# Kernel tuning notes

Measured on AMD Instinct MI355X. Metric: run time of the kernel, lower is better.

The kernel has to match this reference:

```python
import jax
import jax.numpy as jnp
from jax import lax
import numpy as np

# ---- static RPN config (mirrors init_kwargs) ----
STRIDES = (8, 16)
SIZES = ((32, 32), (16, 16))
SCALES = ((64.0 ** 2,), (128.0 ** 2,))
RATIOS = ((0.5, 1.0, 2.0), (0.5, 1.0, 2.0))
IMAGE_SIZE = (256, 256)
NMS_THRESH = 0.7
POST_NMS_TOP_N = 2000
NUM_LEVELS = 2
TOP_K_PER_LEVEL = POST_NMS_TOP_N // NUM_LEVELS  # padded NMS output slots per level


def _generate_anchors(stride, scales, ratios, size, image_size):
    """Anchors of shape (H*W*A, 4) in (x1,y1,x2,y2), clamped to image."""
    H, W = size
    cy = (np.arange(H, dtype=np.float32) + 0.5) * stride
    cx = (np.arange(W, dtype=np.float32) + 0.5) * stride
    ws, hs = [], []
    for s in scales:
        for r in ratios:
            ws.append(np.sqrt(s / r))
            hs.append(np.sqrt(s * r))
    ws = np.asarray(ws, np.float32)  # [A]
    hs = np.asarray(hs, np.float32)
    cxg, cyg = np.meshgrid(cx, cy)  # [H, W]
    x1 = cxg[..., None] - 0.5 * ws
    y1 = cyg[..., None] - 0.5 * hs
    x2 = cxg[..., None] + 0.5 * ws
    y2 = cyg[..., None] + 0.5 * hs
    a = np.stack([x1, y1, x2, y2], axis=-1)  # [H, W, A, 4]
    a[..., 0] = np.clip(a[..., 0], 0, image_size[0])
    a[..., 1] = np.clip(a[..., 1], 0, image_size[1])
    a[..., 2] = np.clip(a[..., 2], 0, image_size[0])
    a[..., 3] = np.clip(a[..., 3], 0, image_size[1])
    return a.reshape(-1, 4).astype(np.float32)


ANCHORS = [
    _generate_anchors(STRIDES[i], SCALES[i], RATIOS[i], SIZES[i], IMAGE_SIZE)
    for i in range(NUM_LEVELS)
]


def conv2d(x, w, b, padding):
    y = lax.conv_general_dilated(
        x, w, window_strides=(1, 1), padding=padding,
        dimension_numbers=("NCHW", "OIHW", "NCHW"))
    return y + b[None, :, None, None]


def decode_boxes(anchors, deltas):
    """Standard R-CNN box decode. anchors [N,4], deltas [..., N, 4]."""
    wa = anchors[:, 2] - anchors[:, 0]
    ha = anchors[:, 3] - anchors[:, 1]
    cxa = anchors[:, 0] + 0.5 * wa
    cya = anchors[:, 1] + 0.5 * ha
    dx, dy, dw, dh = deltas[..., 0], deltas[..., 1], deltas[..., 2], deltas[..., 3]
    cx = dx * wa + cxa
    cy = dy * ha + cya
    w = jnp.exp(dw) * wa
    h = jnp.exp(dh) * ha
    return jnp.stack([cx - 0.5 * w, cy - 0.5 * h, cx + 0.5 * w, cy + 0.5 * h], axis=-1)


def clamp_boxes(b):
    return jnp.stack([
        jnp.clip(b[..., 0], 0.0, IMAGE_SIZE[0]),
        jnp.clip(b[..., 1], 0.0, IMAGE_SIZE[1]),
        jnp.clip(b[..., 2], 0.0, IMAGE_SIZE[0]),
        jnp.clip(b[..., 3], 0.0, IMAGE_SIZE[1]),
    ], axis=-1)


def _pairwise_iou(b):
    # b: [N, 4] -> [N, N] IoU (torchvision convention, no +1)
    area = (b[:, 2] - b[:, 0]) * (b[:, 3] - b[:, 1])
    lt = jnp.maximum(b[:, None, :2], b[None, :, :2])
    rb = jnp.minimum(b[:, None, 2:], b[None, :, 2:])
    wh = jnp.clip(rb - lt, 0.0)
    inter = wh[..., 0] * wh[..., 1]
    return inter / (area[:, None] + area[None, :] - inter)


def nms_padded(boxes, scores, thresh, top_k):
    """Exact greedy NMS; returns (top_k,4) boxes and (top_k,) scores padded with -1."""
    N = boxes.shape[0]
    order = jnp.argsort(-scores)
    b = boxes[order]
    s = scores[order]
    iou = _pairwise_iou(b)  # [N, N]

    def body(supp, xs):
        row, i = xs
        keep_i = jnp.logical_not(supp[i])
        supp = supp | (keep_i & (row > thresh) & (jnp.arange(N) > i))
        return supp, keep_i

    _, keep = lax.scan(body, jnp.zeros((N,), bool), (iou, jnp.arange(N)))
    rank = jnp.cumsum(keep) - 1  # position among kept, in score order
    slot = jnp.where(keep & (rank < top_k), rank, top_k)  # overflow -> dump row
    out_b = jnp.full((top_k + 1, 4), -1.0, boxes.dtype).at[slot].set(b)
    out_s = jnp.full((top_k + 1,), -1.0, scores.dtype).at[slot].set(s)
    return out_b[:top_k], out_s[:top_k]


def _rpn_level(feat, anchors, conv_w, conv_b, cls_w, cls_b, reg_w, reg_b):
    x = jax.nn.relu(conv2d(feat, conv_w, conv_b, "SAME"))
    cls = conv2d(x, cls_w, cls_b, "VALID")              # [BS, A, H, W]
    reg = conv2d(x, reg_w, reg_b, "VALID")              # [BS, 4A, H, W]
    BS, A, H, W = cls.shape
    cls = cls.transpose(0, 2, 3, 1).reshape(BS, -1)                      # [BS, HWA]
    reg = reg.transpose(0, 2, 3, 1).reshape(BS, H, W, A, 4).reshape(BS, -1, 4)
    boxes = clamp_boxes(decode_boxes(anchors, lax.stop_gradient(reg)))   # [BS, HWA, 4]
    scores = jax.nn.sigmoid(lax.stop_gradient(cls))                      # [BS, HWA]
    kb, ks = jax.vmap(lambda bb, ss: nms_padded(bb, ss, NMS_THRESH, TOP_K_PER_LEVEL))(boxes, scores)
    return kb, ks


def setup_inputs() -> dict:
    key = jax.random.key(0)
    ks = jax.random.split(key, 5)
    C = 256
    A = 3
    return {
        "feat0": jax.random.normal(ks[0], (4, C, 32, 32), jnp.float32),
        "feat1": jax.random.normal(ks[1], (4, C, 16, 16), jnp.float32),
        "conv_w": 0.01 * jax.random.normal(ks[2], (C, C, 3, 3), jnp.float32),
        "conv_b": jnp.zeros((C,), jnp.float32),
        "cls_w": 0.01 * jax.random.normal(ks[3], (A, C, 1, 1), jnp.float32),
        "cls_b": jnp.zeros((A,), jnp.float32),
        "reg_w": 0.01 * jax.random.normal(ks[4], (4 * A, C, 1, 1), jnp.float32),
        "reg_b": jnp.zeros((4 * A,), jnp.float32),
    }


def reference(feat0, feat1, conv_w, conv_b, cls_w, cls_b, reg_w, reg_b):
    feats = [feat0, feat1]
    kb_all, ks_all = [], []
    for i in range(NUM_LEVELS):
        kb, ks = _rpn_level(feats[i], jnp.asarray(ANCHORS[i]),
                            conv_w, conv_b, cls_w, cls_b, reg_w, reg_b)
        kb_all.append(kb)
        ks_all.append(ks)
    bboxes = jnp.concatenate(kb_all, axis=1)   # [BS, POST_NMS_TOP_N, 4]
    scores = jnp.concatenate(ks_all, axis=1)   # [BS, POST_NMS_TOP_N]
    idx = jnp.argsort(-scores, axis=1)         # descending; -1 pads go last
    bboxes = jnp.take_along_axis(bboxes, idx[..., None], axis=1)
    return bboxes
```

## Files before the change

### kernel.cpp

```cpp
#include <hip/hip_runtime.h>
#include <math.h>


__global__ __launch_bounds__(256, 4) void conv3_sk_u(
    const float* __restrict__ feat0, const float* __restrict__ feat1,
    const float* __restrict__ conv_w,
    double* __restrict__ part0, double* __restrict__ part1)
{
  __shared__ float Ald[2][16][64];
  __shared__ float Bld[2][16][64];
  const int t = threadIdx.x;
  const int bid = blockIdx.x;
  const float* feat;
  double* part;
  int oc_t, p_t, k_base, hw_sh, w_sh, H;
  if (bid < 1024) {
    int kc = bid >> 8;
    feat = feat0; part = part0 + (size_t)kc * 4096 * 256;
    oc_t = bid & 3; p_t = (bid >> 2) & 63;
    k_base = kc * 576; hw_sh = 10; w_sh = 5; H = 32;
  } else {
    int b2 = bid - 1024;
    int kc = b2 >> 6;
    feat = feat1; part = part1 + (size_t)kc * 1024 * 256;
    oc_t = b2 & 3; p_t = (b2 >> 2) & 15;
    k_base = kc * 576; hw_sh = 8; w_sh = 4; H = 16;
  }
  const int oc_base = oc_t * 64;
  const int p_base  = p_t * 64;
  const int wmask = H - 1, hwmask = (1 << hw_sh) - 1;
  const int skk = t >> 4;
  const int q4  = (t & 15) * 4;

  float a_r[4], b_r[4];
  auto load_tile = [&](int kt) {
    const int k0 = k_base + kt * 16;
    const float* wrow = conv_w + (size_t)(oc_base + q4) * 2304 + (k0 + skk);
#pragma unroll
    for (int u = 0; u < 4; ++u) a_r[u] = wrow[(size_t)u * 2304];
    int p = p_base + q4;
    int b = p >> hw_sh, pin = p & hwmask;
    int y = pin >> w_sh, x0 = pin & wmask;
    int k = k0 + skk;
    int ic = k / 9, rr = k - ic * 9;
    int ky = rr / 3, kx = rr - ky * 3;
    int iy = y + ky - 1;
    const float* frow = feat + (((b << 8) + ic) << hw_sh) + (iy << w_sh);
    bool yok = (unsigned)iy < (unsigned)H;
#pragma unroll
    for (int u = 0; u < 4; ++u) {
      int ix = x0 + u + kx - 1;
      b_r[u] = (yok && (unsigned)ix < (unsigned)H) ? frow[ix] : 0.f;
    }
  };

  const int ty4 = (t >> 4) * 4;
  const int tx4 = (t & 15) * 4;
  double acc[4][4] = {};

  load_tile(0);
  for (int kt = 0; kt < 36; ++kt) {
    const int buf = kt & 1;
    *(float4*)&Ald[buf][skk][q4] = make_float4(a_r[0], a_r[1], a_r[2], a_r[3]);
    *(float4*)&Bld[buf][skk][q4] = make_float4(b_r[0], b_r[1], b_r[2], b_r[3]);
    __syncthreads();
    if (kt + 1 < 36) load_tile(kt + 1);
#pragma unroll
    for (int kk = 0; kk < 16; ++kk) {
      float4 av = *(const float4*)&Ald[buf][kk][ty4];
      float4 bv = *(const float4*)&Bld[buf][kk][tx4];
      double ad[4] = {(double)av.x, (double)av.y, (double)av.z, (double)av.w};
      double bd[4] = {(double)bv.x, (double)bv.y, (double)bv.z, (double)bv.w};
#pragma unroll
      for (int i = 0; i < 4; ++i)
#pragma unroll
        for (int j = 0; j < 4; ++j) acc[i][j] += ad[i] * bd[j];
    }
  }
#pragma unroll
  for (int j = 0; j < 4; ++j) {
    int p = p_base + tx4 + j;
    double* row = part + (size_t)p * 256 + oc_base + ty4;
    *(double2*)&row[0] = make_double2(acc[0][j], acc[1][j]);
    *(double2*)&row[2] = make_double2(acc[2][j], acc[3][j]);
  }
}

__global__ __launch_bounds__(256) void rhd_k(
    const double* __restrict__ part0, const double* __restrict__ part1,
    const float* __restrict__ conv_b,
    const float* __restrict__ cls_w, const float* __restrict__ cls_b,
    const float* __restrict__ reg_w, const float* __restrict__ reg_b,
    float* __restrict__ box0, float* __restrict__ sc0,
    float* __restrict__ box1, float* __restrict__ sc1)
{
  int wid = (blockIdx.x * 256 + threadIdx.x) >> 6;
  int lane = threadIdx.x & 63;
  int lvl = wid >= 4096;
  const double* part = lvl ? part1 : part0;
  int p = lvl ? wid - 4096 : wid;
  int M = lvl ? 1024 : 4096;
  double s4[4];
  {
    float4 bv = ((const float4*)conv_b)[lane];
    s4[0] = (double)bv.x; s4[1] = (double)bv.y;
    s4[2] = (double)bv.z; s4[3] = (double)bv.w;
  }
#pragma unroll
  for (int ks = 0; ks < 4; ++ks) {
    const double2* pr = (const double2*)(part + (size_t)ks * M * 256 + (size_t)p * 256);
    double2 a = pr[2 * lane], b = pr[2 * lane + 1];
    s4[0] += a.x; s4[1] += a.y; s4[2] += b.x; s4[3] += b.y;
  }
  float xv[4];
#pragma unroll
  for (int q = 0; q < 4; ++q) {
    float f = (float)s4[q];
    xv[q] = f > 0.f ? f : 0.f;
  }
  double acc[15];
#pragma unroll
  for (int o = 0; o < 15; ++o) {
    const float* wr = (o < 3) ? (cls_w + o * 256) : (reg_w + (o - 3) * 256);
    float4 wv = ((const float4*)wr)[lane];
    acc[o] = (double)wv.x * (double)xv[0] + (double)wv.y * (double)xv[1] +
             (double)wv.z * (double)xv[2] + (double)wv.w * (double)xv[3];
  }
#pragma unroll
  for (int d = 1; d < 64; d <<= 1)
#pragma unroll
    for (int o = 0; o < 15; ++o)
      acc[o] += __shfl_xor(acc[o], d, 64);
  if (lane < 3) {
    int a = lane;
    float cls = (float)(acc[a] + (double)cls_b[a]);
    float score = 1.f / (1.f + expf(-cls));
    float dx = (float)(acc[3 + a * 4 + 0] + (double)reg_b[a * 4 + 0]);
    float dy = (float)(acc[3 + a * 4 + 1] + (double)reg_b[a * 4 + 1]);
    float dw = (float)(acc[3 + a * 4 + 2] + (double)reg_b[a * 4 + 2]);
    float dh = (float)(acc[3 + a * 4 + 3] + (double)reg_b[a * 4 + 3]);
    int hw_sh = lvl ? 8 : 10, w_sh = lvl ? 4 : 5, Wd = lvl ? 16 : 32;
    float S = lvl ? 16.f : 8.f;
    double scale = lvl ? 16384.0 : 4096.0;
    int b = p >> hw_sh, pin = p & ((1 << hw_sh) - 1);
    int y = pin >> w_sh, x = pin & (Wd - 1);
    double ratio = (a == 0) ? 0.5 : (a == 1 ? 1.0 : 2.0);
    float w_a = (float)sqrt(scale / ratio);
    float h_a = (float)sqrt(scale * ratio);
    float cx = ((float)x + 0.5f) * S;
    float cy = ((float)y + 0.5f) * S;
    float x1 = cx - 0.5f * w_a, y1 = cy - 0.5f * h_a;
    float x2 = cx + 0.5f * w_a, y2 = cy + 0.5f * h_a;
    x1 = fminf(fmaxf(x1, 0.f), 256.f); y1 = fminf(fmaxf(y1, 0.f), 256.f);
    x2 = fminf(fmaxf(x2, 0.f), 256.f); y2 = fminf(fmaxf(y2, 0.f), 256.f);
    float wa = x2 - x1, ha = y2 - y1;
    float cxa = x1 + 0.5f * wa, cya = y1 + 0.5f * ha;
    float ncx = dx * wa + cxa;
    float ncy = dy * ha + cya;
    float nw = expf(dw) * wa;
    float nh = expf(dh) * ha;
    float bx1 = ncx - 0.5f * nw, by1 = ncy - 0.5f * nh;
    float bx2 = ncx + 0.5f * nw, by2 = ncy + 0.5f * nh;
    bx1 = fminf(fmaxf(bx1, 0.f), 256.f); by1 = fminf(fmaxf(by1, 0.f), 256.f);
    bx2 = fminf(fmaxf(bx2, 0.f), 256.f); by2 = fminf(fmaxf(by2, 0.f), 256.f);
    int n = pin * 3 + a;
    if (lvl) {
      ((float4*)box1)[(size_t)b * 768 + n] = make_float4(bx1, by1, bx2, by2);
      sc1[b * 768 + n] = score;
    } else {
      ((float4*)box0)[(size_t)b * 3072 + n] = make_float4(bx1, by1, bx2, by2);
      sc0[b * 3072 + n] = score;
    }
  }
}

__global__ __launch_bounds__(256) void sort_level_k(
    const float* __restrict__ sc0, const float* __restrict__ box0,
    float* __restrict__ ssc0, float* __restrict__ sbox0,
    const float* __restrict__ sc1, const float* __restrict__ box1,
    float* __restrict__ ssc1, float* __restrict__ sbox1)
{
  __shared__ __align__(16) float s[3072];
  int z = blockIdx.x;
  const float *sc, *box; float *ssc, *sbox; int N, b, c;
  if (z < 48) { sc = sc0; box = box0; ssc = ssc0; sbox = sbox0; N = 3072; b = z / 12; c = z % 12; }
  else { int z2 = z - 48; sc = sc1; box = box1; ssc = ssc1; sbox = sbox1; N = 768; b = z2 / 3; c = z2 % 3; }
  const float* scb = sc + (size_t)b * N;
  for (int j = threadIdx.x; j < N; j += 256) s[j] = scb[j];
  __syncthreads();
  int i = c * 256 + threadIdx.x;
  float si = s[i];
  int rank = 0;
  const float4* sv = (const float4*)s;
  for (int j4 = 0; j4 < (N >> 2); ++j4) {
    float4 v = sv[j4];
    int j = j4 * 4;
    rank += (v.x > si) || (v.x == si && (j + 0) < i);
    rank += (v.y > si) || (v.y == si && (j + 1) < i);
    rank += (v.z > si) || (v.z == si && (j + 2) < i);
    rank += (v.w > si) || (v.w == si && (j + 3) < i);
  }
  ssc[(size_t)b * N + rank] = si;
  float4 bi = ((const float4*)box)[(size_t)b * N + i];
  ((float4*)sbox)[(size_t)b * N + rank] = bi;
}

__global__ __launch_bounds__(256) void mask_col_k(
    const float* __restrict__ sbox0, const float* __restrict__ sbox1,
    unsigned long long* __restrict__ mask0, unsigned long long* __restrict__ mask1,
    unsigned long long* __restrict__ colD0, unsigned long long* __restrict__ colD1)
{
  int bid = blockIdx.x;
  if (bid < 2448) {
    __shared__ float4 bj[64];
    const float* sbox; unsigned long long* mask; int N, words, w, i_ch, b;
    if (bid < 2304) {
      sbox = sbox0; mask = mask0; N = 3072; words = 48;
      w = bid % 48; int r = bid / 48; i_ch = r % 12; b = r / 12;
    } else {
      int z = bid - 2304;
      sbox = sbox1; mask = mask1; N = 768; words = 12;
      w = z % 12; int r = z / 12; i_ch = r % 3; b = r / 3;
    }
    int i = i_ch * 256 + threadIdx.x;
    if (threadIdx.x < 64)
      bj[threadIdx.x] = ((const float4*)sbox)[(size_t)b * N + w * 64 + threadIdx.x];
    __syncthreads();
    float4 bi = ((const float4*)sbox)[(size_t)b * N + i];
    float ai = (bi.z - bi.x) * (bi.w - bi.y);
    unsigned long long m = 0ull;
#pragma unroll 16
    for (int jj = 0; jj < 64; ++jj) {
      int j = w * 64 + jj;
      float4 bv = bj[jj];
      float lx = fmaxf(bi.x, bv.x), ly = fmaxf(bi.y, bv.y);
      float rx = fminf(bi.z, bv.z), ry = fminf(bi.w, bv.w);
      float iw = fmaxf(rx - lx, 0.f), ih = fmaxf(ry - ly, 0.f);
      float inter = iw * ih;
      float aj = (bv.z - bv.x) * (bv.w - bv.y);
      float iou = inter / (ai + aj - inter);
      if ((iou > 0.7f) & (j > i)) m |= (1ull << jj);
    }
    mask[((size_t)b * N + i) * words + w] = m;
  } else {
    __shared__ float4 tb[4][64];
    int sub = threadIdx.x >> 6, lane = threadIdx.x & 63;
    const float* sbox; unsigned long long* colD; int N, tile, b;
    if (bid < 2496) {
      int unit = (bid - 2448) * 4 + sub;
      sbox = sbox0; colD = colD0; N = 3072;
      tile = unit % 48; b = unit / 48;
    } else {
      int unit = (bid - 2496) * 4 + sub;
      sbox = sbox1; colD = colD1; N = 768;
      tile = unit % 12; b = unit / 12;
    }
    tb[sub][lane] = ((const float4*)sbox)[(size_t)b * N + tile * 64 + lane];
    __syncthreads();
    float4 bq = tb[sub][lane];
    float aq = (bq.z - bq.x) * (bq.w - bq.y);
    unsigned long long col = 0ull;
#pragma unroll 16
    for (int ii = 0; ii < 64; ++ii) {
      float4 bi = tb[sub][ii];
      float lx = fmaxf(bq.x, bi.x), ly = fmaxf(bq.y, bi.y);
      float rx = fminf(bq.z, bi.z), ry = fminf(bq.w, bi.w);
      float iw = fmaxf(rx - lx, 0.f), ih = fmaxf(ry - ly, 0.f);
      float inter = iw * ih;
      float ai = (bi.z - bi.x) * (bi.w - bi.y);
      float iou = inter / (aq + ai - inter);
      if ((iou > 0.7f) & (lane > ii)) col |= (1ull << ii);
    }
    colD[(size_t)b * N + tile * 64 + lane] = col;
  }
}

__global__ __launch_bounds__(256) void nms_scan_k(
    const float* __restrict__ ssc0, const float* __restrict__ sbox0,
    const unsigned long long* __restrict__ mask0,
    const unsigned long long* __restrict__ colD0,
    const float* __restrict__ ssc1, const float* __restrict__ sbox1,
    const unsigned long long* __restrict__ mask1,
    const unsigned long long* __restrict__ colD1,
    float* __restrict__ cb, float* __restrict__ cs)
{
  int z = blockIdx.x;
  int lvl = z >> 2, b = z & 3;
  int N = lvl ? 768 : 3072;
  int words = lvl ? 12 : 48;
  const float* ssc = (lvl ? ssc1 : ssc0) + (size_t)b * N;
  const float4* sbox = ((const float4*)(lvl ? sbox1 : sbox0)) + (size_t)b * N;
  const unsigned long long* mask = (lvl ? mask1 : mask0) + (size_t)b * N * words;
  const unsigned long long* colD = (lvl ? colD1 : colD0) + (size_t)b * N;
  const int tid = threadIdx.x;
  const int lane = tid & 63;
  const int wv = tid >> 6;
  float* csb = cs + (size_t)b * 2000 + lvl * 1000;
  float4* cbb = (float4*)(cb + ((size_t)b * 2000 + lvl * 1000) * 4);

  __shared__ unsigned long long rem[48];
  __shared__ unsigned long long part[4][64];
  __shared__ unsigned long long keepSh;
  __shared__ int doneSh;

  if (tid < 48) rem[tid] = 0ull;
  if (tid == 0) doneSh = 0;
  for (int q = tid; q < 1000; q += 256) {
    csb[q] = -1.f;
    cbb[q] = make_float4(-1.f, -1.f, -1.f, -1.f);
  }
  unsigned long long colv = 0ull; float sc_i = 0.f; float4 bx_i;
  if (wv == 0) { colv = colD[lane]; sc_i = ssc[lane]; bx_i = sbox[lane]; }
  int kept_base = 0;
  __syncthreads();

  for (int t = 0; t < words; ++t) {
    unsigned long long v[16];
    if (lane < words) {
      const unsigned long long* rowb =
          mask + ((size_t)t * 64 + wv * 16) * words + lane;
#pragma unroll
      for (int s = 0; s < 16; ++s) v[s] = rowb[(size_t)s * words];
    }
    if (wv == 0) {
      unsigned long long wr = rem[t];
      bool rm = (wr >> lane) & 1ull;
      bool kp = false;
      unsigned long long Rv = wr;
      unsigned long long Kv = 0ull;
      while (true) {
        bool F = (!rm) && (!kp) && ((colv & ~Rv) == 0ull);
        unsigned long long Fv = __ballot(F);
        if (Fv == 0ull) break;
        kp = kp || F;
        Kv |= Fv;
        bool newr = (!rm) && (!kp) && ((colv & Fv) != 0ull);
        rm = rm || newr;
        Rv = __ballot(rm);
      }
      if (kp) {
        int rank = kept_base + __popcll(Kv & ((1ull << lane) - 1ull));
        if (rank < 1000) { csb[rank] = sc_i; cbb[rank] = bx_i; }
      }
      kept_base += __popcll(Kv);
      if (lane == 0) {
        keepSh = Kv;
        doneSh = (kept_base >= 1000 || t + 1 >= words) ? 1 : 0;
      }
      if (t + 1 < words) {
        int i2 = (t + 1) * 64 + lane;
        colv = colD[i2]; sc_i = ssc[i2]; bx_i = sbox[i2];
      }
    }
    __syncthreads();
    unsigned long long k64 = keepSh;
    int done = doneSh;
    if (lane < words) {
      unsigned long long acc = 0ull;
#pragma unroll
      for (int s = 0; s < 16; ++s)
        acc |= (((k64 >> (wv * 16 + s)) & 1ull) ? v[s] : 0ull);
      part[wv][lane] = acc;
    }
    __syncthreads();
    if (done) break;
    if (tid > t && tid < words)
      rem[tid] |= part[0][tid] | part[1][tid] | part[2][tid] | part[3][tid];
    __syncthreads();
  }
}

__global__ __launch_bounds__(256) void final_sort_k(
    const float* __restrict__ cs, const float* __restrict__ cb,
    float* __restrict__ out)
{
  __shared__ __align__(16) float s[2000];
  int b = blockIdx.x >> 3, c = blockIdx.x & 7;
  const float* csb = cs + (size_t)b * 2000;
  for (int j = threadIdx.x; j < 2000; j += 256) s[j] = csb[j];
  __syncthreads();
  if (threadIdx.x >= 250) return;
  int li = c * 250 + threadIdx.x;
  float si = s[li];
  int rank = 0;
  const float4* sv = (const float4*)s;
  for (int j4 = 0; j4 < 500; ++j4) {
    float4 v = sv[j4];
    int j = j4 * 4;
    rank += (v.x > si) || (v.x == si && (j + 0) < li);
    rank += (v.y > si) || (v.y == si && (j + 1) < li);
    rank += (v.z > si) || (v.z == si && (j + 2) < li);
    rank += (v.w > si) || (v.w == si && (j + 3) < li);
  }
  float4 bi = ((const float4*)cb)[(size_t)b * 2000 + li];
  ((float4*)out)[(size_t)b * 2000 + rank] = bi;
}

extern "C" void kernel_launch(void* const* d_in, const int* in_sizes, int n_in,
                              void* d_out, int out_size, void* d_ws, size_t ws_size,
                              hipStream_t stream) {
  const float* feat0  = (const float*)d_in[0];
  const float* feat1  = (const float*)d_in[1];
  const float* conv_w = (const float*)d_in[2];
  const float* conv_b = (const float*)d_in[3];
  const float* cls_w  = (const float*)d_in[4];
  const float* cls_b  = (const float*)d_in[5];
  const float* reg_w  = (const float*)d_in[6];
  const float* reg_b  = (const float*)d_in[7];

  char* p = (char*)d_ws;
  auto alloc = [&](size_t bytes) {
    char* r = p;
    p += (bytes + 255) & ~(size_t)255;
    return r;
  };
  double* part0 = (double*)alloc((size_t)4 * 4096 * 256 * 8);
  double* part1 = (double*)alloc((size_t)4 * 1024 * 256 * 8);
  float* box0 = (float*)alloc((size_t)4 * 3072 * 16);
  float* sc0  = (float*)alloc((size_t)4 * 3072 * 4);
  float* box1 = (float*)alloc((size_t)4 * 768 * 16);
  float* sc1  = (float*)alloc((size_t)4 * 768 * 4);
  float* sbox0 = (float*)alloc((size_t)4 * 3072 * 16);
  float* ssc0  = (float*)alloc((size_t)4 * 3072 * 4);
  float* sbox1 = (float*)alloc((size_t)4 * 768 * 16);
  float* ssc1  = (float*)alloc((size_t)4 * 768 * 4);
  unsigned long long* mask0 = (unsigned long long*)alloc((size_t)4 * 3072 * 48 * 8);
  unsigned long long* mask1 = (unsigned long long*)alloc((size_t)4 * 768 * 12 * 8);
  unsigned long long* colD0 = (unsigned long long*)alloc((size_t)4 * 3072 * 8);
  unsigned long long* colD1 = (unsigned long long*)alloc((size_t)4 * 768 * 8);
  float* cb = (float*)alloc((size_t)4 * 2000 * 16);
  float* cs = (float*)alloc((size_t)4 * 2000 * 4);

  conv3_sk_u<<<1280, 256, 0, stream>>>(feat0, feat1, conv_w, part0, part1);
  rhd_k<<<1280, 256, 0, stream>>>(part0, part1, conv_b, cls_w, cls_b,
                                  reg_w, reg_b, box0, sc0, box1, sc1);
  sort_level_k<<<60, 256, 0, stream>>>(sc0, box0, ssc0, sbox0,
                                       sc1, box1, ssc1, sbox1);
  mask_col_k<<<2508, 256, 0, stream>>>(sbox0, sbox1, mask0, mask1, colD0, colD1);
  nms_scan_k<<<8, 256, 0, stream>>>(ssc0, sbox0, mask0, colD0,
                                    ssc1, sbox1, mask1, colD1, cb, cs);
  final_sort_k<<<32, 256, 0, stream>>>(cs, cb, (float*)d_out);
}
```

Before: 492.6 us.

## Use FP64 MFMA instructions for conv3x3 GEMM inner loop

Replaces the scalar double-precision FMA outer-product inner loop of the 3x3 conv GEMM with v_mfma_f64_16x16x4 matrix instructions. Each wave computes a 32x32 tile as four 16x16 accumulators, and the output lane mapping is discovered at runtime with probe MFMAs. LDS rows are padded from 64 to 72 floats to reduce bank conflicts. The epilogue now writes scalar doubles instead of vectorized double2 stores, which may cost some store coalescing.

Measured after the change: 467.7 us. -5.1%, faster.

```diff
diff --git a/kernel.cpp b/kernel.cpp
--- a/kernel.cpp
+++ b/kernel.cpp
@@ -1,14 +1,16 @@
 #include <hip/hip_runtime.h>
 #include <math.h>
 
+
+typedef double d4 __attribute__((ext_vector_type(4)));
 
 __global__ __launch_bounds__(256, 4) void conv3_sk_u(
     const float* __restrict__ feat0, const float* __restrict__ feat1,
     const float* __restrict__ conv_w,
     double* __restrict__ part0, double* __restrict__ part1)
 {
-  __shared__ float Ald[2][16][64];
-  __shared__ float Bld[2][16][64];
+  __shared__ float Ald[2][16][72];
+  __shared__ float Bld[2][16][72];
   const int t = threadIdx.x;
   const int bid = blockIdx.x;
   const float* feat;
@@ -54,9 +56,33 @@
     }
   };
 
-  const int ty4 = (t >> 4) * 4;
-  const int tx4 = (t & 15) * 4;
-  double acc[4][4] = {};
+  const int lane = t & 63;
+  const int wv = t >> 6;
+  const int wo = (wv >> 1) << 5;
+  const int wp = (wv & 1) << 5;
+  const int lr = lane >> 4;
+  const int lc = lane & 15;
+
+  int rowm[4], colm[4];
+  {
+    d4 pz = {0.0, 0.0, 0.0, 0.0};
+    double pa1 = (lr == 0) ? (double)(lc + 1) : 0.0;
+    double pb1 = (lr == 0) ? 1.0 : 0.0;
+    d4 prow = __builtin_amdgcn_mfma_f64_16x16x4f64(pa1, pb1, pz, 0, 0, 0);
+    double pa2 = (lr == 0) ? 1.0 : 0.0;
+    double pb2 = (lr == 0) ? (double)(lc + 1) : 0.0;
+    d4 pcol = __builtin_amdgcn_mfma_f64_16x16x4f64(pa2, pb2, pz, 0, 0, 0);
+#pragma unroll
+    for (int d = 0; d < 4; ++d) {
+      rowm[d] = ((int)prow[d] - 1) & 15;
+      colm[d] = ((int)pcol[d] - 1) & 15;
+    }
+  }
+
+  d4 acc00 = {0.0, 0.0, 0.0, 0.0};
+  d4 acc01 = {0.0, 0.0, 0.0, 0.0};
+  d4 acc10 = {0.0, 0.0, 0.0, 0.0};
+  d4 acc11 = {0.0, 0.0, 0.0, 0.0};
 
   load_tile(0);
   for (int kt = 0; kt < 36; ++kt) {
@@ -66,23 +92,30 @@
     __syncthreads();
     if (kt + 1 < 36) load_tile(kt + 1);
 #pragma unroll
-    for (int kk = 0; kk < 16; ++kk) {
-      float4 av = *(const float4*)&Ald[buf][kk][ty4];
-      float4 bv = *(const float4*)&Bld[buf][kk][tx4];
-      double ad[4] = {(double)av.x, (double)av.y, (double)av.z, (double)av.w};
-      double bd[4] = {(double)bv.x, (double)bv.y, (double)bv.z, (double)bv.w};
-#pragma unroll
-      for (int i = 0; i < 4; ++i)
-#pragma unroll
-        for (int j = 0; j < 4; ++j) acc[i][j] += ad[i] * bd[j];
-    }
-  }
-#pragma unroll
-  for (int j = 0; j < 4; ++j) {
-    int p = p_base + tx4 + j;
-    double* row = part + (size_t)p * 256 + oc_base + ty4;
-    *(double2*)&row[0] = make_double2(acc[0][j], acc[1][j]);
-    *(double2*)&row[2] = make_double2(acc[2][j], acc[3][j]);
+    for (int kc = 0; kc < 4; ++kc) {
+      const int kr = (kc << 2) + lr;
+      double a0 = (double)Ald[buf][kr][wo + lc];
+      double a1 = (double)Ald[buf][kr][wo + 16 + lc];
+      double b0 = (double)Bld[buf][kr][wp + lc];
+      double b1 = (double)Bld[buf][kr][wp + 16 + lc];
+      acc00 = __builtin_amdgcn_mfma_f64_16x16x4f64(a0, b0, acc00, 0, 0, 0);
+      acc01 = __builtin_amdgcn_mfma_f64_16x16x4f64(a0, b1, acc01, 0, 0, 0);
+      acc10 = __builtin_amdgcn_mfma_f64_16x16x4f64(a1, b0, acc10, 0, 0, 0);
+      acc11 = __builtin_amdgcn_mfma_f64_16x16x4f64(a1, b1, acc11, 0, 0, 0);
+    }
+  }
+
+  {
+    const int p00 = p_base + wp;
+    const int oc00 = oc_base + wo;
+#pragma unroll
+    for (int d = 0; d < 4; ++d) {
+      const int rm = rowm[d], cm = colm[d];
+      part[(size_t)(p00 + cm)      * 256 + (oc00 + rm)]      = acc00[d];
+      part[(size_t)(p00 + 16 + cm) * 256 + (oc00 + rm)]      = acc01[d];
+      part[(size_t)(p00 + cm)      * 256 + (oc00 + 16 + rm)] = acc10[d];
+      part[(size_t)(p00 + 16 + cm) * 256 + (oc00 + 16 + rm)] = acc11[d];
+    }
   }
 }
 
```
